# Kernel tuning notes

Hardware: AMD Instinct MI355X
Metric: run time of the kernel (lower is better)

## Reference

```python
import jax, jax.numpy as jnp
import numpy as np

NEG_SLOPE = 0.01  # torch leaky_relu default


def _conv1x3(x, w, b):
    # x: (B, C_in, N, T), w: (C_out, C_in, 1, 3) -> (B, C_out, N, T-2)
    y = jax.lax.conv_general_dilated(x, w, window_strides=(1, 1), padding='VALID',
                                     dimension_numbers=('NCHW', 'OIHW', 'NCHW'))
    return y + b[None, :, None, None]


def _timeblock(X, cw1, cb1, cw2, cb2, cw3, cb3):
    # X: (B, N, T, C_in) -> (B, N, T-2, C_out)
    x = jnp.transpose(X, (0, 3, 1, 2))
    temp = _conv1x3(x, cw1, cb1) + jax.nn.sigmoid(_conv1x3(x, cw2, cb2))
    out = jax.nn.relu(temp + _conv1x3(x, cw3, cb3))
    return jnp.transpose(out, (0, 2, 3, 1))


def setup_inputs() -> dict:
    key = jax.random.key(0)
    ks = jax.random.split(key, 10)
    B, N, T, Cin, Cout = 8, 2048, 64, 16, 4
    att_dim = T - 2  # 62
    D = att_dim * Cout  # 248 per node; fc in_features = 2*D = 496
    X = jax.random.normal(ks[0], (B, N, T, Cin), dtype=jnp.float32)
    # sparse-ish binary adjacency
    A = jax.random.randint(ks[1], (N, N), 0, 2).astype(jnp.float32)
    s = 0.05
    cw1 = jax.random.normal(ks[2], (Cout, Cin, 1, 3), dtype=jnp.float32) * s
    cb1 = jax.random.normal(ks[3], (Cout,), dtype=jnp.float32) * s
    cw2 = jax.random.normal(ks[4], (Cout, Cin, 1, 3), dtype=jnp.float32) * s
    cb2 = jax.random.normal(ks[5], (Cout,), dtype=jnp.float32) * s
    cw3 = jax.random.normal(ks[6], (Cout, Cin, 1, 3), dtype=jnp.float32) * s
    cb3 = jax.random.normal(ks[7], (Cout,), dtype=jnp.float32) * s
    fcw = jax.random.normal(ks[8], (2 * D,), dtype=jnp.float32) * s
    fcb = jax.random.normal(ks[9], (), dtype=jnp.float32) * s
    return {"X": X, "A": A, "cw1": cw1, "cb1": cb1, "cw2": cw2, "cb2": cb2,
            "cw3": cw3, "cb3": cb3, "fcw": fcw, "fcb": fcb}


def reference(X, A, cw1, cb1, cw2, cb2, cw3, cb3, fcw, fcb):
    t = _timeblock(X, cw1, cb1, cw2, cb2, cw3, cb3)  # (B, N, T-2, 4)
    B, N, To, C = t.shape
    D = To * C
    tf = t.reshape(B, N, D)
    wi, wj = fcw[:D], fcw[D:]
    si = tf @ wi  # (B, N) contribution of source node i
    sj = tf @ wj  # (B, N) contribution of target node j
    scores = jax.nn.leaky_relu(si[:, :, None] + sj[:, None, :] + fcb, NEG_SLOPE)
    mask = (A != 0.0)[None]  # entries for zero edges stay 0 before softmax
    att = jnp.where(mask, scores, 0.0)
    soft = jax.nn.softmax(att, axis=2)
    return soft * A[None]
```

## Files before the change

### kernel.cpp

```cpp
#include <hip/hip_runtime.h>
#include <cfloat>

#define N_NODES 2048
#define BN_TOTAL 16384

__global__ __launch_bounds__(256) void k_sisj(
    const float* __restrict__ X,
    const float* __restrict__ cw1, const float* __restrict__ cb1,
    const float* __restrict__ cw2, const float* __restrict__ cb2,
    const float* __restrict__ cw3, const float* __restrict__ cb3,
    const float* __restrict__ fcw,
    float* __restrict__ si, float* __restrict__ sj)
{
    __shared__ float Xs[64 * 20];
    __shared__ float Ws[3 * 192];
    __shared__ float Bs[12];
    __shared__ float red[8];

    const int tid = threadIdx.x;
    const int bn  = blockIdx.x;

    {
        const float4 v = ((const float4*)(X + (size_t)bn * 1024))[tid];
        const int g = tid * 4, row = g >> 4, col = g & 15;
        *(float4*)&Xs[row * 20 + col] = v;
    }
    if (tid < 192) {
        const int c = tid / 48, rem = tid % 48, ci = rem / 3, dt = rem % 3;
        const int d = c * 48 + dt * 16 + ci;
        Ws[d]       = cw1[tid];
        Ws[192 + d] = cw2[tid];
        Ws[384 + d] = cw3[tid];
    }
    if (tid < 12) Bs[tid] = tid < 4 ? cb1[tid] : (tid < 8 ? cb2[tid - 4] : cb3[tid - 8]);
    __syncthreads();

    const int to = tid >> 2, c = tid & 3;
    float t_val = 0.f;
    if (to < 62) {
        float4 xr[3][4];
        #pragma unroll
        for (int dt = 0; dt < 3; ++dt)
            #pragma unroll
            for (int q = 0; q < 4; ++q)
                xr[dt][q] = *(const float4*)&Xs[(to + dt) * 20 + q * 4];

        float acc[3];
        #pragma unroll
        for (int k = 0; k < 3; ++k) {
            float a = Bs[k * 4 + c];
            #pragma unroll
            for (int dt = 0; dt < 3; ++dt)
                #pragma unroll
                for (int q = 0; q < 4; ++q) {
                    const float4 w = *(const float4*)&Ws[k * 192 + c * 48 + dt * 16 + q * 4];
                    a = fmaf(xr[dt][q].x, w.x, a);
                    a = fmaf(xr[dt][q].y, w.y, a);
                    a = fmaf(xr[dt][q].z, w.z, a);
                    a = fmaf(xr[dt][q].w, w.w, a);
                }
            acc[k] = a;
        }
        const float sig = 1.f / (1.f + __expf(-acc[1]));
        const float tv  = acc[0] + sig + acc[2];
        t_val = tv > 0.f ? tv : 0.f;
    }

    float a = 0.f, b = 0.f;
    if (tid < 248) { a = t_val * fcw[tid]; b = t_val * fcw[248 + tid]; }
    #pragma unroll
    for (int off = 32; off > 0; off >>= 1) {
        a += __shfl_down(a, off);
        b += __shfl_down(b, off);
    }
    const int wid = tid >> 6;
    if ((tid & 63) == 0) { red[wid] = a; red[4 + wid] = b; }
    __syncthreads();
    if (tid == 0) {
        si[bn] = red[0] + red[1] + red[2] + red[3];
        sj[bn] = red[4] + red[5] + red[6] + red[7];
    }
}

__global__ __launch_bounds__(256) void k_att(
    const float* __restrict__ A,
    const float* __restrict__ si, const float* __restrict__ sj,
    const float* __restrict__ fcb,
    float* __restrict__ out)
{
    __shared__ float redm[4];
    __shared__ float reds[4];

    const int row = blockIdx.x;
    const int b   = row >> 11;
    const int i   = row & (N_NODES - 1);
    const int tid = threadIdx.x;

    const float cbase = si[row] + fcb[0];
    const float* __restrict__ sjb = sj + b * N_NODES;
    const float* __restrict__ Ar  = A + (size_t)i * N_NODES;

    float avv[8], att[8];
    float m = -FLT_MAX;
    #pragma unroll
    for (int u = 0; u < 2; ++u) {
        const int j4 = tid + u * 256;
        const float4 a4 = ((const float4*)Ar)[j4];
        const float4 s4 = ((const float4*)sjb)[j4];
        const float aa[4] = {a4.x, a4.y, a4.z, a4.w};
        const float ss[4] = {s4.x, s4.y, s4.z, s4.w};
        #pragma unroll
        for (int q = 0; q < 4; ++q) {
            float s = cbase + ss[q];
            s = (s >= 0.f) ? s : 0.01f * s;
            const float at_ = (aa[q] != 0.f) ? s : 0.f;
            avv[u * 4 + q] = aa[q];
            att[u * 4 + q] = at_;
            m = fmaxf(m, at_);
        }
    }

    #pragma unroll
    for (int off = 32; off > 0; off >>= 1) m = fmaxf(m, __shfl_xor(m, off));
    if ((tid & 63) == 0) redm[tid >> 6] = m;
    __syncthreads();
    m = fmaxf(fmaxf(redm[0], redm[1]), fmaxf(redm[2], redm[3]));

    float sum = 0.f;
    #pragma unroll
    for (int u = 0; u < 8; ++u) { att[u] = __expf(att[u] - m); sum += att[u]; }

    #pragma unroll
    for (int off = 32; off > 0; off >>= 1) sum += __shfl_xor(sum, off);
    if ((tid & 63) == 0) reds[tid >> 6] = sum;
    __syncthreads();
    sum = reds[0] + reds[1] + reds[2] + reds[3];

    const float inv = 1.f / sum;
    float* __restrict__ orow = out + (size_t)row * N_NODES;
    #pragma unroll
    for (int u = 0; u < 2; ++u) {
        const int j4 = tid + u * 256;
        float4 o;
        o.x = avv[u * 4 + 0] * (att[u * 4 + 0] * inv);
        o.y = avv[u * 4 + 1] * (att[u * 4 + 1] * inv);
        o.z = avv[u * 4 + 2] * (att[u * 4 + 2] * inv);
        o.w = avv[u * 4 + 3] * (att[u * 4 + 3] * inv);
        ((float4*)orow)[j4] = o;
    }
}

extern "C" void kernel_launch(void* const* d_in, const int* in_sizes, int n_in,
                              void* d_out, int out_size, void* d_ws, size_t ws_size,
                              hipStream_t stream)
{
    const float* X   = (const float*)d_in[0];
    const float* A   = (const float*)d_in[1];
    const float* cw1 = (const float*)d_in[2];
    const float* cb1 = (const float*)d_in[3];
    const float* cw2 = (const float*)d_in[4];
    const float* cb2 = (const float*)d_in[5];
    const float* cw3 = (const float*)d_in[6];
    const float* cb3 = (const float*)d_in[7];
    const float* fcw = (const float*)d_in[8];
    const float* fcb = (const float*)d_in[9];
    float* out = (float*)d_out;

    float* si = (float*)d_ws;
    float* sj = si + BN_TOTAL;

    hipLaunchKernelGGL(k_sisj, dim3(BN_TOTAL), dim3(256), 0, stream,
                       X, cw1, cb1, cw2, cb2, cw3, cb3, fcw, si, sj);
    hipLaunchKernelGGL(k_att, dim3(BN_TOTAL), dim3(256), 0, stream,
                       A, si, sj, fcb, out);
}
```

Before: 229.4 us.

## Process two nodes per conv block, drop softmax max pass, remap rows per XCD

The time-block kernel now handles two nodes per block, with each wavefront owning one output channel and reading its weights directly instead of staging them in shared memory. The attention kernel skips the row-max reduction and its barrier, exponentiating scores directly. It also remaps block indices so each XCD processes a contiguous range of adjacency rows across batches for better L2 reuse of A, and writes output with nontemporal stores. Removing the max subtraction risks overflow if scores become large.

Result: faster. 223.8 us (-2.4%).

```diff
diff --git a/kernel.cpp b/kernel.cpp
--- a/kernel.cpp
+++ b/kernel.cpp
@@ -3,6 +3,8 @@
 
 #define N_NODES 2048
 #define BN_TOTAL 16384
+
+typedef float vf4 __attribute__((ext_vector_type(4)));
 
 __global__ __launch_bounds__(256) void k_sisj(
     const float* __restrict__ X,
@@ -12,73 +14,95 @@
     const float* __restrict__ fcw,
     float* __restrict__ si, float* __restrict__ sj)
 {
-    __shared__ float Xs[64 * 20];
-    __shared__ float Ws[3 * 192];
-    __shared__ float Bs[12];
-    __shared__ float red[8];
+    __shared__ float tile[2][1024];
+    __shared__ float red[4][2][2];
 
-    const int tid = threadIdx.x;
-    const int bn  = blockIdx.x;
+    const int tid  = threadIdx.x;
+    const int wid  = tid >> 6;
+    const int lane = tid & 63;
+    const int bn0  = blockIdx.x * 2;
 
     {
-        const float4 v = ((const float4*)(X + (size_t)bn * 1024))[tid];
-        const int g = tid * 4, row = g >> 4, col = g & 15;
-        *(float4*)&Xs[row * 20 + col] = v;
+        const vf4 v0 = *(const vf4*)(X + (size_t)bn0 * 1024 + tid * 4);
+        const vf4 v1 = *(const vf4*)(X + (size_t)(bn0 + 1) * 1024 + tid * 4);
+        *(vf4*)&tile[0][tid * 4] = v0;
+        *(vf4*)&tile[1][tid * 4] = v1;
     }
-    if (tid < 192) {
-        const int c = tid / 48, rem = tid % 48, ci = rem / 3, dt = rem % 3;
-        const int d = c * 48 + dt * 16 + ci;
-        Ws[d]       = cw1[tid];
-        Ws[192 + d] = cw2[tid];
-        Ws[384 + d] = cw3[tid];
-    }
-    if (tid < 12) Bs[tid] = tid < 4 ? cb1[tid] : (tid < 8 ? cb2[tid - 4] : cb3[tid - 8]);
     __syncthreads();
 
-    const int to = tid >> 2, c = tid & 3;
-    float t_val = 0.f;
+    const int c_u = __builtin_amdgcn_readfirstlane(wid);
+    const float* __restrict__ w1 = cw1 + c_u * 48;
+    const float* __restrict__ w2 = cw2 + c_u * 48;
+    const float* __restrict__ w3 = cw3 + c_u * 48;
+    const float b1 = cb1[c_u], b2 = cb2[c_u], b3 = cb3[c_u];
+
+    const int to = lane;
+    float t0 = 0.f, t1 = 0.f;
+
     if (to < 62) {
-        float4 xr[3][4];
+        vf4 xr0[3][4], xr1[3][4];
         #pragma unroll
         for (int dt = 0; dt < 3; ++dt)
             #pragma unroll
-            for (int q = 0; q < 4; ++q)
-                xr[dt][q] = *(const float4*)&Xs[(to + dt) * 20 + q * 4];
+            for (int q = 0; q < 4; ++q) {
+                xr0[dt][q] = *(const vf4*)&tile[0][(to + dt) * 16 + q * 4];
+                xr1[dt][q] = *(const vf4*)&tile[1][(to + dt) * 16 + q * 4];
+            }
+        const float* xf0 = (const float*)xr0;
+        const float* xf1 = (const float*)xr1;
 
-        float acc[3];
+        float acc0[3] = {b1, b2, b3};
+        float acc1[3] = {b1, b2, b3};
+        const float* __restrict__ wp[3] = {w1, w2, w3};
         #pragma unroll
         for (int k = 0; k < 3; ++k) {
-            float a = Bs[k * 4 + c];
+            float wk[48];
             #pragma unroll
-            for (int dt = 0; dt < 3; ++dt)
+            for (int q = 0; q < 12; ++q)
+                *(vf4*)&wk[q * 4] = *(const vf4*)(wp[k] + q * 4);
+            float a0 = acc0[k], a1 = acc1[k];
+            #pragma unroll
+            for (int ci = 0; ci < 16; ++ci)
                 #pragma unroll
-                for (int q = 0; q < 4; ++q) {
-                    const float4 w = *(const float4*)&Ws[k * 192 + c * 48 + dt * 16 + q * 4];
-                    a = fmaf(xr[dt][q].x, w.x, a);
-                    a = fmaf(xr[dt][q].y, w.y, a);
-                    a = fmaf(xr[dt][q].z, w.z, a);
-                    a = fmaf(xr[dt][q].w, w.w, a);
+                for (int dt = 0; dt < 3; ++dt) {
+                    const float w = wk[ci * 3 + dt];
+                    a0 = fmaf(xf0[dt * 16 + ci], w, a0);
+                    a1 = fmaf(xf1[dt * 16 + ci], w, a1);
                 }
-            acc[k] = a;
+            acc0[k] = a0; acc1[k] = a1;
         }
-        const float sig = 1.f / (1.f + __expf(-acc[1]));
-        const float tv  = acc[0] + sig + acc[2];
-        t_val = tv > 0.f ? tv : 0.f;
+        const float s0 = 1.f / (1.f + __expf(-acc0[1]));
+        const float s1 = 1.f / (1.f + __expf(-acc1[1]));
+        const float v0 = acc0[0] + s0 + acc0[2];
+        const float v1 = acc1[0] + s1 + acc1[2];
+        t0 = v0 > 0.f ? v0 : 0.f;
+        t1 = v1 > 0.f ? v1 : 0.f;
     }
 
-    float a = 0.f, b = 0.f;
-    if (tid < 248) { a = t_val * fcw[tid]; b = t_val * fcw[248 + tid]; }
+    float pi0 = 0.f, pj0 = 0.f, pi1 = 0.f, pj1 = 0.f;
+    if (to < 62) {
+        const float wi = fcw[to * 4 + c_u];
+        const float wj = fcw[248 + to * 4 + c_u];
+        pi0 = t0 * wi; pj0 = t0 * wj;
+        pi1 = t1 * wi; pj1 = t1 * wj;
+    }
     #pragma unroll
     for (int off = 32; off > 0; off >>= 1) {
-        a += __shfl_down(a, off);
-        b += __shfl_down(b, off);
+        pi0 += __shfl_xor(pi0, off);
+        pj0 += __shfl_xor(pj0, off);
+        pi1 += __shfl_xor(pi1, off);
+        pj1 += __shfl_xor(pj1, off);
     }
-    const int wid = tid >> 6;
-    if ((tid & 63) == 0) { red[wid] = a; red[4 + wid] = b; }
+    if (lane == 0) {
+        red[wid][0][0] = pi0; red[wid][0][1] = pj0;
+        red[wid][1][0] = pi1; red[wid][1][1] = pj1;
+    }
     __syncthreads();
-    if (tid == 0) {
-        si[bn] = red[0] + red[1] + red[2] + red[3];
-        sj[bn] = red[4] + red[5] + red[6] + red[7];
+    if (tid < 4) {
+        const int n = tid >> 1, cmp = tid & 1;
+        const float s = red[0][n][cmp] + red[1][n][cmp] + red[2][n][cmp] + red[3][n][cmp];
+        float* __restrict__ dst = cmp ? sj : si;
+        dst[bn0 + n] = s;
     }
 }
 
@@ -88,47 +112,38 @@
     const float* __restrict__ fcb,
     float* __restrict__ out)
 {
-    __shared__ float redm[4];
     __shared__ float reds[4];
 
-    const int row = blockIdx.x;
-    const int b   = row >> 11;
-    const int i   = row & (N_NODES - 1);
-    const int tid = threadIdx.x;
+    const int blk   = blockIdx.x;
+    const int xcd   = blk & 7;
+    const int local = blk >> 3;
+    const int i     = (xcd << 8) | (local & 255);
+    const int b     = local >> 8;
+    const int row   = b * N_NODES + i;
+    const int tid   = threadIdx.x;
 
     const float cbase = si[row] + fcb[0];
     const float* __restrict__ sjb = sj + b * N_NODES;
     const float* __restrict__ Ar  = A + (size_t)i * N_NODES;
 
     float avv[8], att[8];
-    float m = -FLT_MAX;
+    float sum = 0.f;
     #pragma unroll
     for (int u = 0; u < 2; ++u) {
         const int j4 = tid + u * 256;
-        const float4 a4 = ((const float4*)Ar)[j4];
-        const float4 s4 = ((const float4*)sjb)[j4];
-        const float aa[4] = {a4.x, a4.y, a4.z, a4.w};
-        const float ss[4] = {s4.x, s4.y, s4.z, s4.w};
+        const vf4 a4 = ((const vf4*)Ar)[j4];
+        const vf4 s4 = ((const vf4*)sjb)[j4];
         #pragma unroll
         for (int q = 0; q < 4; ++q) {
-            float s = cbase + ss[q];
+            float s = cbase + s4[q];
             s = (s >= 0.f) ? s : 0.01f * s;
-            const float at_ = (aa[q] != 0.f) ? s : 0.f;
-            avv[u * 4 + q] = aa[q];
-            att[u * 4 + q] = at_;
-            m = fmaxf(m, at_);
+            const float at_ = (a4[q] != 0.f) ? s : 0.f;
+            const float e = __expf(at_);
+            avv[u * 4 + q] = a4[q];
+            att[u * 4 + q] = e;
+            sum += e;
         }
     }
-
-    #pragma unroll
-    for (int off = 32; off > 0; off >>= 1) m = fmaxf(m, __shfl_xor(m, off));
-    if ((tid & 63) == 0) redm[tid >> 6] = m;
-    __syncthreads();
-    m = fmaxf(fmaxf(redm[0], redm[1]), fmaxf(redm[2], redm[3]));
-
-    float sum = 0.f;
-    #pragma unroll
-    for (int u = 0; u < 8; ++u) { att[u] = __expf(att[u] - m); sum += att[u]; }
 
     #pragma unroll
     for (int off = 32; off > 0; off >>= 1) sum += __shfl_xor(sum, off);
@@ -141,12 +156,12 @@
     #pragma unroll
     for (int u = 0; u < 2; ++u) {
         const int j4 = tid + u * 256;
-        float4 o;
-        o.x = avv[u * 4 + 0] * (att[u * 4 + 0] * inv);
-        o.y = avv[u * 4 + 1] * (att[u * 4 + 1] * inv);
-        o.z = avv[u * 4 + 2] * (att[u * 4 + 2] * inv);
-        o.w = avv[u * 4 + 3] * (att[u * 4 + 3] * inv);
-        ((float4*)orow)[j4] = o;
+        vf4 o;
+        o[0] = avv[u * 4 + 0] * (att[u * 4 + 0] * inv);
+        o[1] = avv[u * 4 + 1] * (att[u * 4 + 1] * inv);
+        o[2] = avv[u * 4 + 2] * (att[u * 4 + 2] * inv);
+        o[3] = avv[u * 4 + 3] * (att[u * 4 + 3] * inv);
+        __builtin_nontemporal_store(o, (vf4*)orow + j4);
     }
 }
 
@@ -169,7 +184,7 @@
     float* si = (float*)d_ws;
     float* sj = si + BN_TOTAL;
 
-    hipLaunchKernelGGL(k_sisj, dim3(BN_TOTAL), dim3(256), 0, stream,
+    hipLaunchKernelGGL(k_sisj, dim3(BN_TOTAL / 2), dim3(256), 0, stream,
                        X, cw1, cb1, cw2, cb2, cw3, cb3, fcw, si, sj);
     hipLaunchKernelGGL(k_att, dim3(BN_TOTAL), dim3(256), 0, stream,
                        A, si, sj, fcb, out);
```
